# Performance work log

Measured on AMD Instinct MI355X. Metric: run time of the kernel, lower is better.

Reference implementation:

```python
import jax, jax.numpy as jnp
import numpy as np

B, S, D, H, HD = 1, 2048, 1024, 16, 64
GH = 64            # GammaGate hidden dim
FFN_H = int(D * 4 * 2 / 3)
CTX = 512          # omega-rule context window c
LAM = 0.999        # base exponential decay

def _rms(x, w, eps=1e-6):
    return x * jax.lax.rsqrt(jnp.mean(x * x, axis=-1, keepdims=True) + eps) * w

def _rope(q, k):
    hd = q.shape[-1]; s = q.shape[2]
    inv = 1.0 / (10000.0 ** (jnp.arange(0, hd, 2, dtype=jnp.float32) / hd))
    fr = jnp.arange(s, dtype=jnp.float32)[:, None] * inv[None, :]
    cos = jnp.concatenate([jnp.cos(fr), jnp.cos(fr)], -1)
    sin = jnp.concatenate([jnp.sin(fr), jnp.sin(fr)], -1)
    rot = lambda x: jnp.concatenate([-x[..., hd // 2:], x[..., :hd // 2]], -1)
    return q * cos + rot(q) * sin, k * cos + rot(k) * sin

def setup_inputs() -> dict:
    key = jax.random.key(0)
    ks = jax.random.split(key, 10)
    n = lambda i, sh, s=0.02: jax.random.normal(ks[i], sh, jnp.float32) * s
    return dict(
        x=jax.random.normal(ks[0], (B, S, D), jnp.float32),
        norm1_w=jnp.ones((D,), jnp.float32),
        norm2_w=jnp.ones((D,), jnp.float32),
        w_qkv=n(1, (D, 3 * D)),
        q_norm_w=jnp.ones((HD,), jnp.float32),
        k_norm_w=jnp.ones((HD,), jnp.float32),
        gamma_w1=n(2, (D, GH)),
        gamma_w2=n(3, (GH, 1)),
        m_persist=n(4, (H, HD, HD)),
        memory_gate=jnp.array([-3.0], jnp.float32),
        w_o=n(5, (D, D), 0.02 / 2 ** 0.5),
        ffn_w1=n(6, (D, FFN_H)),
        ffn_w3=n(7, (D, FFN_H)),
        ffn_w2=n(8, (FFN_H, D)),
    )

def reference(x, norm1_w, norm2_w, w_qkv, q_norm_w, k_norm_w, gamma_w1, gamma_w2,
              m_persist, memory_gate, w_o, ffn_w1, ffn_w3, ffn_w2):
    b, s, d = x.shape
    h = _rms(x, norm1_w)
    qkv = h @ w_qkv
    q, k, v = jnp.split(qkv, 3, axis=-1)
    rs = lambda t: t.reshape(b, s, H, HD).transpose(0, 2, 1, 3)   # (b,h,s,hd)
    q, k, v = rs(q), rs(k), rs(v)
    q = _rms(q, q_norm_w); k = _rms(k, k_norm_w)                  # qk_norm
    q, k = _rope(q, k)
    # input-dependent gamma gate: Linear->SiLU->Linear->Sigmoid
    gamma = jax.nn.sigmoid(jax.nn.silu(h @ gamma_w1) @ gamma_w2)  # (b,s,1)
    # Omega-rule memory: Q'_t = (M_p q_t + sum_i w_{t,i} k_i (k_i . q_t)) / (1 + sum_i w_{t,i})
    ti = jnp.arange(s)
    delta = ti[:, None] - ti[None, :]
    wmask = (delta >= 0) & (delta < CTX)
    decay = jnp.where(wmask, LAM ** delta.astype(jnp.float32), 0.0)      # (t,i)
    w = decay[None, None] * gamma[:, None, None, :, 0]                   # (b,1,t,i)
    norm = 1.0 + jnp.sum(w, axis=-1)                                     # (b,1,t)
    scores = jnp.einsum('bhtd,bhid->bhti', q, k)
    contrib = jnp.einsum('bhti,bhid->bhtd', w * scores, k)
    persist = jnp.einsum('hde,bhte->bhtd', m_persist, q)
    qp = (persist + contrib) / norm[..., None]
    gate = jax.nn.sigmoid(memory_gate)[0]
    q = (1.0 - gate) * q + gate * qp
    # causal attention
    aw = jnp.einsum('bhtd,bhid->bhti', q, k) * (HD ** -0.5)
    causal = ti[:, None] >= ti[None, :]
    aw = jnp.where(causal[None, None], aw, -jnp.inf)
    aw = jax.nn.softmax(aw, axis=-1)
    ao = jnp.einsum('bhti,bhid->bhtd', aw, v).transpose(0, 2, 1, 3).reshape(b, s, d)
    x = x + ao @ w_o
    h2 = _rms(x, norm2_w)
    x = x + (jax.nn.silu(h2 @ ffn_w1) * (h2 @ ffn_w3)) @ ffn_w2   # SwiGLU
    return x
```

## Files before the change

### kernel.cpp

```cpp
#include <hip/hip_runtime.h>
#include <hip/hip_bf16.h>

#define S_LEN 2048
#define D_DIM 1024
#define H_NUM 16
#define HD_DIM 64
#define GH_DIM 64
#define FFN_H 2730
#define FFNP  2816
#define CTX_W 512
#define L2LAM -0.00144341687f
#define QBLK 64
#define KBLK 64
#define ALDK 76
#define QSCALE 0.1803368801111731f

typedef unsigned short u16;
typedef __attribute__((ext_vector_type(8))) short bf16x8_t;
typedef __attribute__((ext_vector_type(4))) float f32x4_t;

__device__ inline float wave_sum(float v) {
    for (int off = 32; off; off >>= 1) v += __shfl_xor(v, off);
    return v;
}
__device__ inline u16 f2bf(float f) {
    unsigned r;
    asm("v_cvt_pk_bf16_f32 %0, %1, %2" : "=v"(r) : "v"(f), "v"(f));
    return (u16)r;
}
__device__ inline unsigned f2bf2(float lo, float hi) {
    unsigned r;
    asm("v_cvt_pk_bf16_f32 %0, %1, %2" : "=v"(r) : "v"(lo), "v"(hi));
    return r;
}
__device__ inline float bf2f(u16 u) {
    return __uint_as_float(((unsigned int)u) << 16);
}
__device__ inline void gload16(const void* g, void* l) {
    __builtin_amdgcn_global_load_lds(
        (const __attribute__((address_space(1))) void*)g,
        (__attribute__((address_space(3))) void*)l, 16, 0, 0);
}

__global__ __launch_bounds__(256) void rmsnorm_kernel(
    const float* __restrict__ in, const float* __restrict__ w,
    u16* __restrict__ out)
{
    __shared__ float wsum[4];
    int row = blockIdx.x;
    int tid = threadIdx.x, lane = tid & 63, wv = tid >> 6;
    const float4* ir = reinterpret_cast<const float4*>(in + (size_t)row * D_DIM);
    float4 v = ir[tid];
    float ss = v.x*v.x + v.y*v.y + v.z*v.z + v.w*v.w;
    ss = wave_sum(ss);
    if (lane == 0) wsum[wv] = ss;
    __syncthreads();
    float tot = wsum[0] + wsum[1] + wsum[2] + wsum[3];
    float scale = rsqrtf(tot / (float)D_DIM + 1e-6f);
    const float4* wr = reinterpret_cast<const float4*>(w);
    float4 wv4 = wr[tid];
    uint2 o;
    o.x = f2bf2(v.x * scale * wv4.x, v.y * scale * wv4.y);
    o.y = f2bf2(v.z * scale * wv4.z, v.w * scale * wv4.w);
    *reinterpret_cast<uint2*>(out + (size_t)row * D_DIM + tid * 4) = o;
}

__global__ __launch_bounds__(256) void prep_kernel(
    const float* __restrict__ w_qkv, const float* __restrict__ w_o,
    const float* __restrict__ w1f, const float* __restrict__ w3f,
    const float* __restrict__ w2f, const float* __restrict__ gw1f,
    u16* __restrict__ wqT, u16* __restrict__ woT, u16* __restrict__ w13T,
    u16* __restrict__ w2T, u16* __restrict__ gw1T,
    const float* __restrict__ x, const float* __restrict__ norm1_w,
    u16* __restrict__ h_bf)
{
    __shared__ float tile[64][65];
    __shared__ float wsum[4];
    int b = blockIdx.x;
    int tid = threadIdx.x;
    if (b < 3152) {
        const float* src; u16* dst;
        int srcK, srcN, Kp, rowOff, rowMul, nbx;
        if (b < 768)       {           src = w_qkv; dst = wqT;  srcK = 1024; srcN = 3072; Kp = 1024; rowOff = 0; rowMul = 1; nbx = 48; }
        else if (b < 1024) { b -= 768;  src = w_o;  dst = woT;  srcK = 1024; srcN = 1024; Kp = 1024; rowOff = 0; rowMul = 1; nbx = 16; }
        else if (b < 1728) { b -= 1024; src = w1f;  dst = w13T; srcK = 1024; srcN = 2730; Kp = 1024; rowOff = 0; rowMul = 2; nbx = 44; }
        else if (b < 2432) { b -= 1728; src = w3f;  dst = w13T; srcK = 1024; srcN = 2730; Kp = 1024; rowOff = 1; rowMul = 2; nbx = 44; }
        else if (b < 3136) { b -= 2432; src = w2f;  dst = w2T;  srcK = 2730; srcN = 1024; Kp = 2816; rowOff = 0; rowMul = 1; nbx = 16; }
        else               { b -= 3136; src = gw1f; dst = gw1T; srcK = 1024; srcN = 64;   Kp = 1024; rowOff = 0; rowMul = 1; nbx = 1; }
        int n0 = (b % nbx) * 64, k0 = (b / nbx) * 64;
        int tx = tid & 15, ty = tid >> 4;
        bool interior = (k0 + 63 < srcK) && (n0 + 63 < srcN);
        #pragma unroll
        for (int p = 0; p < 4; ++p) {
            int kk = p * 16 + ty;
            int r = k0 + kk;
            int cb = n0 + tx * 4;
            float4 v;
            if (interior) {
                v = *(const float4*)(src + (size_t)r * srcN + cb);
            } else {
                v.x = (r < srcK && cb     < srcN) ? src[(size_t)r * srcN + cb]     : 0.f;
                v.y = (r < srcK && cb + 1 < srcN) ? src[(size_t)r * srcN + cb + 1] : 0.f;
                v.z = (r < srcK && cb + 2 < srcN) ? src[(size_t)r * srcN + cb + 2] : 0.f;
                v.w = (r < srcK && cb + 3 < srcN) ? src[(size_t)r * srcN + cb + 3] : 0.f;
            }
            tile[kk][tx*4+0] = v.x; tile[kk][tx*4+1] = v.y;
            tile[kk][tx*4+2] = v.z; tile[kk][tx*4+3] = v.w;
        }
        __syncthreads();
        int wx = tid & 7, wy = tid >> 3;
        #pragma unroll
        for (int p = 0; p < 2; ++p) {
            int nn = p * 32 + wy;
            int ks = wx * 8;
            uint4 o;
            o.x = f2bf2(tile[ks+0][nn], tile[ks+1][nn]);
            o.y = f2bf2(tile[ks+2][nn], tile[ks+3][nn]);
            o.z = f2bf2(tile[ks+4][nn], tile[ks+5][nn]);
            o.w = f2bf2(tile[ks+6][nn], tile[ks+7][nn]);
            *(uint4*)(dst + (size_t)(rowOff + (size_t)(n0 + nn) * rowMul) * Kp + k0 + ks) = o;
        }
    } else {
        int row = b - 3152;
        int lane = tid & 63, wv = tid >> 6;
        const float4* ir = reinterpret_cast<const float4*>(x + (size_t)row * D_DIM);
        float4 v = ir[tid];
        float ss = v.x*v.x + v.y*v.y + v.z*v.z + v.w*v.w;
        ss = wave_sum(ss);
        if (lane == 0) wsum[wv] = ss;
        __syncthreads();
        float tot = wsum[0] + wsum[1] + wsum[2] + wsum[3];
        float scale = rsqrtf(tot / (float)D_DIM + 1e-6f);
        const float4* wr = reinterpret_cast<const float4*>(norm1_w);
        float4 wv4 = wr[tid];
        uint2 o;
        o.x = f2bf2(v.x * scale * wv4.x, v.y * scale * wv4.y);
        o.y = f2bf2(v.z * scale * wv4.z, v.w * scale * wv4.w);
        *reinterpret_cast<uint2*>(h_bf + (size_t)row * D_DIM + tid * 4) = o;
    }
}

__global__ __launch_bounds__(256) void gamma_gemm_kernel(
    const u16* __restrict__ A, const u16* __restrict__ B,
    const float* __restrict__ w2, float* __restrict__ gamma, int K)
{
    __shared__ u16 As[64 * 64];
    __shared__ u16 Bs[64 * 64];
    __shared__ float red[2][64];
    int tid = threadIdx.x, lane = tid & 63, wid = tid >> 6;
    int wr = wid >> 1, wc = wid & 1;
    int row0 = blockIdx.x * 64;
    int l8 = lane >> 3, l7 = lane & 7;
    f32x4_t acc[2][2];
    #pragma unroll
    for (int i = 0; i < 2; ++i)
        #pragma unroll
        for (int j = 0; j < 2; ++j) acc[i][j] = (f32x4_t)0.f;
    int fr = lane & 15, fo = (lane >> 4) * 8;
    for (int k0 = 0; k0 < K; k0 += 64) {
        #pragma unroll
        for (int i = 0; i < 2; ++i) {
            int ch = wid * 2 + i;
            const u16* ga = A + (size_t)(row0 + ch * 8 + l8) * K + k0 + l7 * 8;
            gload16(ga, &As[ch * 512]);
            const u16* gb = B + (size_t)(ch * 8 + l8) * K + k0 + l7 * 8;
            gload16(gb, &Bs[ch * 512]);
        }
        __syncthreads();
        __builtin_amdgcn_s_setprio(1);
        #pragma unroll
        for (int khf = 0; khf < 2; ++khf) {
            bf16x8_t bfrag[2];
            #pragma unroll
            for (int ni = 0; ni < 2; ++ni)
                bfrag[ni] = *(const bf16x8_t*)&Bs[(wc * 32 + ni * 16 + fr) * 64 + khf * 32 + fo];
            #pragma unroll
            for (int mi = 0; mi < 2; ++mi) {
                bf16x8_t af = *(const bf16x8_t*)&As[(wr * 32 + mi * 16 + fr) * 64 + khf * 32 + fo];
                #pragma unroll
                for (int ni = 0; ni < 2; ++ni)
                    acc[mi][ni] = __builtin_amdgcn_mfma_f32_16x16x32_bf16(
                        af, bfrag[ni], acc[mi][ni], 0, 0, 0);
            }
        }
        __builtin_amdgcn_s_setprio(0);
        __syncthreads();
    }
    int dr = (lane >> 4) * 4, dc = lane & 15;
    float w2v0 = w2[wc * 32 + dc];
    float w2v1 = w2[wc * 32 + 16 + dc];
    #pragma unroll
    for (int mi = 0; mi < 2; ++mi) {
        #pragma unroll
        for (int j = 0; j < 4; ++j) {
            float v0 = acc[mi][0][j];
            float v1 = acc[mi][1][j];
            float t = v0 / (1.f + __expf(-v0)) * w2v0
                    + v1 / (1.f + __expf(-v1)) * w2v1;
            t += __shfl_xor(t, 1);
            t += __shfl_xor(t, 2);
            t += __shfl_xor(t, 4);
            t += __shfl_xor(t, 8);
            if (dc == 0) red[wc][wr * 32 + mi * 16 + dr + j] = t;
        }
    }
    __syncthreads();
    if (tid < 64) {
        float g = red[0][tid] + red[1][tid];
        gamma[row0 + tid] = 1.f / (1.f + __expf(-g));
    }
}

__global__ __launch_bounds__(256) void split_rope_tr_kernel(
    const u16* __restrict__ qkv, const float* __restrict__ qw,
    const float* __restrict__ kw, float* __restrict__ qhp,
    u16* __restrict__ khp, u16* __restrict__ khT, u16* __restrict__ vhT)
{
    __shared__ u16 tk[64][ALDK];
    __shared__ u16 tv[64][ALDK];
    int tid = threadIdx.x;
    int w = tid >> 6, d = tid & 63;
    int h = blockIdx.y;
    int s0 = blockIdx.x * 64;
    float qwv = qw[d], kwv = kw[d];
    int j = d & 31;
    float inv = expf(-(float)j * (9.2103403719761836f / 32.0f));
    float sgn = (d < 32) ? -1.f : 1.f;
    for (int i = 0; i < 16; ++i) {
        int sl = w * 16 + i;
        int s = s0 + sl;
        size_t base = (size_t)s * (3 * D_DIM) + h * HD_DIM + d;
        float qv = bf2f(qkv[base]);
        float kv = bf2f(qkv[base + D_DIM]);
        u16  vv = qkv[base + 2 * D_DIM];
        float sq = wave_sum(qv * qv);
        float qn = qv * rsqrtf(sq / (float)HD_DIM + 1e-6f) * qwv;
        float sk = wave_sum(kv * kv);
        float kn = kv * rsqrtf(sk / (float)HD_DIM + 1e-6f) * kwv;
        float ang = (float)s * inv;
        float cs = cosf(ang), sn = sinf(ang);
        float qp = __shfl_xor(qn, 32);
        float kp = __shfl_xor(kn, 32);
        float qo = qn * cs + sgn * qp * sn;
        float ko = kn * cs + sgn * kp * sn;
        size_t ob = ((size_t)h * S_LEN + s) * HD_DIM + d;
        u16 kb = f2bf(ko);
        qhp[ob] = qo;
        khp[ob] = kb;
        tk[sl][d] = kb;
        tv[sl][d] = vv;
    }
    __syncthreads();
    int r = tid >> 2, cc = (tid & 3) * 16;
    union { u16 u[16]; bf16x8_t v[2]; } ok, ov;
    #pragma unroll
    for (int e = 0; e < 16; ++e) {
        int ksrc = (e & 3) * 16 + (tid & 3) * 4 + (e >> 2);
        ok.u[e] = tk[ksrc][r]; ov.u[e] = tv[ksrc][r];
    }
    u16* kd = khT + ((size_t)h * HD_DIM + r) * S_LEN + s0 + cc;
    u16* vd = vhT + ((size_t)h * HD_DIM + r) * S_LEN + s0 + cc;
    *(bf16x8_t*)kd       = ok.v[0];
    *(bf16x8_t*)(kd + 8) = ok.v[1];
    *(bf16x8_t*)vd       = ov.v[0];
    *(bf16x8_t*)(vd + 8) = ov.v[1];
}

template<int BM, int MODE>
__global__ __launch_bounds__(256) void gemm_bb_kernel(
    const u16* __restrict__ A, const u16* __restrict__ B,
    u16* __restrict__ Cb, int M, int N, int K)
{
    constexpr int MREP = BM / 32;
    constexpr int ACH  = BM / 32;
    __shared__ u16 As[BM * 64];
    __shared__ u16 Bs[128 * 64];
    int tid = threadIdx.x, lane = tid & 63, wid = tid >> 6;
    int wr = wid >> 1, wc = wid & 1;
    int row0 = blockIdx.y * BM, col0 = blockIdx.x * 128;
    int l8 = lane >> 3, l7 = lane & 7;
    f32x4_t acc[MREP][4];
    #pragma unroll
    for (int i = 0; i < MREP; ++i)
        #pragma unroll
        for (int j = 0; j < 4; ++j) acc[i][j] = (f32x4_t)0.f;

    int fr = lane & 15, fo = (lane >> 4) * 8;
    for (int k0 = 0; k0 < K; k0 += 64) {
        #pragma unroll
        for (int i = 0; i < ACH; ++i) {
            int ch = wid * ACH + i;
            const u16* ga = A + (size_t)(row0 + ch * 8 + l8) * K + k0 + l7 * 8;
            gload16(ga, &As[ch * 512]);
        }
        #pragma unroll
        for (int i = 0; i < 4; ++i) {
            int ch = wid * 4 + i;
            const u16* gb = B + (size_t)(col0 + ch * 8 + l8) * K + k0 + l7 * 8;
            gload16(gb, &Bs[ch * 512]);
        }
        __syncthreads();
        __builtin_amdgcn_s_setprio(1);
        #pragma unroll
        for (int khf = 0; khf < 2; ++khf) {
            bf16x8_t bfrag[4];
            #pragma unroll
            for (int ni = 0; ni < 4; ++ni)
                bfrag[ni] = *(const bf16x8_t*)&Bs[(wc * 64 + ni * 16 + fr) * 64 + khf * 32 + fo];
            #pragma unroll
            for (int mi = 0; mi < MREP; ++mi) {
                bf16x8_t af = *(const bf16x8_t*)&As[(wr * (BM / 2) + mi * 16 + fr) * 64 + khf * 32 + fo];
                #pragma unroll
                for (int ni = 0; ni < 4; ++ni)
                    acc[mi][ni] = __builtin_amdgcn_mfma_f32_16x16x32_bf16(
                        af, bfrag[ni], acc[mi][ni], 0, 0, 0);
            }
        }
        __builtin_amdgcn_s_setprio(0);
        __syncthreads();
    }
    int dr = (lane >> 4) * 4, dc = lane & 15;
    #pragma unroll
    for (int mi = 0; mi < MREP; ++mi) {
        int gr = row0 + wr * (BM / 2) + mi * 16 + dr;
        #pragma unroll
        for (int ni = 0; ni < 4; ++ni) {
            int gc = col0 + wc * 64 + ni * 16 + dc;
            #pragma unroll
            for (int j = 0; j < 4; ++j) {
                float v = acc[mi][ni][j];
                if (MODE == 1) {
                    Cb[(size_t)(gr + j) * N + gc] = f2bf(v);
                } else {
                    float partner = __shfl_xor(v, 1);
                    float a1 = (dc & 1) ? partner : v;
                    float a3 = (dc & 1) ? v : partner;
                    float rr = a1 / (1.f + __expf(-a1)) * a3;
                    if (!(dc & 1))
                        Cb[(size_t)(gr + j) * (N >> 1) + (gc >> 1)] = f2bf(rr);
                }
            }
        }
    }
}

__global__ __launch_bounds__(256) void gemm64_kernel(
    const u16* __restrict__ A, const u16* __restrict__ B,
    const float* __restrict__ res, float* __restrict__ Cf,
    int M, int N, int K)
{
    __shared__ u16 As[64 * 64];
    __shared__ u16 Bs[64 * 64];
    int tid = threadIdx.x, lane = tid & 63, wid = tid >> 6;
    int wr = wid >> 1, wc = wid & 1;
    int row0 = blockIdx.y * 64, col0 = blockIdx.x * 64;
    int l8 = lane >> 3, l7 = lane & 7;
    f32x4_t acc[2][2];
    #pragma unroll
    for (int i = 0; i < 2; ++i)
        #pragma unroll
        for (int j = 0; j < 2; ++j) acc[i][j] = (f32x4_t)0.f;
    int fr = lane & 15, fo = (lane >> 4) * 8;
    for (int k0 = 0; k0 < K; k0 += 64) {
        #pragma unroll
        for (int i = 0; i < 2; ++i) {
            int ch = wid * 2 + i;
            const u16* ga = A + (size_t)(row0 + ch * 8 + l8) * K + k0 + l7 * 8;
            gload16(ga, &As[ch * 512]);
            const u16* gb = B + (size_t)(col0 + ch * 8 + l8) * K + k0 + l7 * 8;
            gload16(gb, &Bs[ch * 512]);
        }
        __syncthreads();
        __builtin_amdgcn_s_setprio(1);
        #pragma unroll
        for (int khf = 0; khf < 2; ++khf) {
            bf16x8_t bfrag[2];
            #pragma unroll
            for (int ni = 0; ni < 2; ++ni)
                bfrag[ni] = *(const bf16x8_t*)&Bs[(wc * 32 + ni * 16 + fr) * 64 + khf * 32 + fo];
            #pragma unroll
            for (int mi = 0; mi < 2; ++mi) {
                bf16x8_t af = *(const bf16x8_t*)&As[(wr * 32 + mi * 16 + fr) * 64 + khf * 32 + fo];
                #pragma unroll
                for (int ni = 0; ni < 2; ++ni)
                    acc[mi][ni] = __builtin_amdgcn_mfma_f32_16x16x32_bf16(
                        af, bfrag[ni], acc[mi][ni], 0, 0, 0);
            }
        }
        __builtin_amdgcn_s_setprio(0);
        __syncthreads();
    }
    int dr = (lane >> 4) * 4, dc = lane & 15;
    #pragma unroll
    for (int mi = 0; mi < 2; ++mi) {
        int gr = row0 + wr * 32 + mi * 16 + dr;
        #pragma unroll
        for (int ni = 0; ni < 2; ++ni) {
            int gc = col0 + wc * 32 + ni * 16 + dc;
            #pragma unroll
            for (int j = 0; j < 4; ++j) {
                size_t off = (size_t)(gr + j) * N + gc;
                Cf[off] = acc[mi][ni][j] + res[off];
            }
        }
    }
}

__global__ __launch_bounds__(512) void fused_omega_attn_kernel(
    const float* __restrict__ qhp, const u16* __restrict__ khp,
    const u16* __restrict__ khT, const u16* __restrict__ vhT,
    const float* __restrict__ gammab, const float* __restrict__ mp,
    const float* __restrict__ mg, u16* __restrict__ ao)
{
    __shared__ u16 Ks[2][KBLK][ALDK];
    __shared__ u16 Xt[2][KBLK][ALDK];
    __shared__ u16 Ps[QBLK][ALDK];
    __shared__ float colfL[CTX_W + KBLK];
    __shared__ float redS[2][QBLK];
    const int tid = threadIdx.x, lane = tid & 63, wid = tid >> 6;
    const int wq = wid & 3;
    const int nh = wid >> 2;
    const int b = blockIdx.x;
    const int hi = (b >> 8) & 1;
    const int h = ((b & 7) << 1) + hi;
    const int s5 = (b >> 3) & 31;
    const int qt = hi ? (31 - s5) : s5;
    const int q0 = qt * QBLK;
    const int fr = lane & 15, g4 = lane >> 4;
    const int fko = g4 * 8;
    const int c = fr, rg = g4;
    const int si = tid >> 3, sdb = (tid & 7) * 8;
    const size_t hS = (size_t)h * S_LEN;
    const size_t hD = (size_t)h * HD_DIM;

    int rowt[4]; float rowf[4];
    #pragma unroll
    for (int j = 0; j < 4; ++j) {
        rowt[j] = q0 + wq * 16 + rg * 4 + j;
        rowf[j] = exp2f((float)(wq * 16 + rg * 4 + j) * L2LAM);
    }
    bf16x8_t qf[2];
    {
        const float* qrow = qhp + (hS + q0 + wq * 16 + fr) * HD_DIM;
        #pragma unroll
        for (int u = 0; u < 2; ++u) {
            float4 a = *(const float4*)(qrow + u * 32 + fko);
            float4 bq = *(const float4*)(qrow + u * 32 + fko + 4);
            bf16x8_t f;
            f[0]=f2bf(a.x); f[1]=f2bf(a.y); f[2]=f2bf(a.z); f[3]=f2bf(a.w);
            f[4]=f2bf(bq.x); f[5]=f2bf(bq.y); f[6]=f2bf(bq.z); f[7]=f2bf(bq.w);
            qf[u] = f;
        }
    }
    float qold[2][4];
    #pragma unroll
    for (int nn = 0; nn < 2; ++nn)
        #pragma unroll
        for (int j = 0; j < 4; ++j)
            qold[nn][j] = qhp[(hS + rowt[j]) * HD_DIM + (nh * 2 + nn) * 16 + c];

    f32x4_t accc[2];
    accc[0] = (f32x4_t)0.f; accc[1] = (f32x4_t)0.f;
    float wsum[4] = {0.f, 0.f, 0.f, 0.f};
    const int kt0 = (q0 > (CTX_W - 1)) ? (q0 - (CTX_W - 1)) / KBLK : 0;
    const int i0 = kt0 * KBLK;
    const int nwin = (qt + 1) * KBLK - i0;
    for (int idx = tid; idx < nwin; idx += 512) {
        int icol = i0 + idx;
        colfL[idx] = exp2f((float)(q0 - icol) * L2LAM) * gammab[icol];
    }
    {
        const u16* gk = khp + (hS + kt0 * KBLK + si) * HD_DIM + sdb;
        const u16* gx = khT + (hD + si) * S_LEN + kt0 * KBLK + sdb;
        *(bf16x8_t*)&Ks[0][si][sdb] = *(const bf16x8_t*)gk;
        *(bf16x8_t*)&Xt[0][si][sdb] = *(const bf16x8_t*)gx;
    }
    __syncthreads();
    int cur = 0;
    for (int kt = kt0; kt <= qt; ++kt) {
        const int k0 = kt * KBLK;
        const bool hn = (kt < qt);
        bf16x8_t nk0, nx0;
        if (hn) {
            const u16* gk = khp + (hS + k0 + KBLK + si) * HD_DIM + sdb;
            const u16* gx = khT + (hD + si) * S_LEN + k0 + KBLK + sdb;
            nk0 = *(const bf16x8_t*)gk;
            nx0 = *(const bf16x8_t*)gx;
        }
        f32x4_t s[2];
        s[0] = (f32x4_t)0.f; s[1] = (f32x4_t)0.f;
        __builtin_amdgcn_s_setprio(1);
        #pragma unroll
        for (int u = 0; u < 2; ++u)
            #pragma unroll
            for (int nn = 0; nn < 2; ++nn) {
                bf16x8_t kb = *(const bf16x8_t*)&Ks[cur][(nh * 2 + nn) * 16 + fr][u * 32 + fko];
                s[nn] = __builtin_amdgcn_mfma_f32_16x16x32_bf16(qf[u], kb, s[nn], 0, 0, 0);
            }
        __builtin_amdgcn_s_setprio(0);
        const bool boundary = (kt == kt0) || (kt == qt);
        float colf[2];
        #pragma unroll
        for (int nn = 0; nn < 2; ++nn)
            colf[nn] = colfL[k0 - i0 + (nh * 2 + nn) * 16 + c];
        #pragma unroll
        for (int j = 0; j < 4; ++j) {
            float pv[2];
            #pragma unroll
            for (int nn = 0; nn < 2; ++nn) {
                float w;
                if (boundary) {
                    int delta = rowt[j] - (k0 + (nh * 2 + nn) * 16 + c);
                    w = (delta >= 0 && delta < CTX_W) ? rowf[j] * colf[nn] : 0.f;
                } else {
                    w = rowf[j] * colf[nn];
                }
                wsum[j] += w;
                pv[nn] = w * s[nn][j];
            }
            *(unsigned*)&Ps[wq * 16 + rg * 4 + j][c * 4 + nh * 2] = f2bf2(pv[0], pv[1]);
        }
        __syncthreads();
        __builtin_amdgcn_s_setprio(1);
        #pragma unroll
        for (int u = 0; u < 2; ++u) {
            bf16x8_t pa = *(const bf16x8_t*)&Ps[wq * 16 + fr][u * 32 + fko];
            #pragma unroll
            for (int nn = 0; nn < 2; ++nn) {
                bf16x8_t kb = *(const bf16x8_t*)&Xt[cur][(nh * 2 + nn) * 16 + fr][u * 32 + fko];
                accc[nn] = __builtin_amdgcn_mfma_f32_16x16x32_bf16(pa, kb, accc[nn], 0, 0, 0);
            }
        }
        __builtin_amdgcn_s_setprio(0);
        if (hn) {
            int nxt = cur ^ 1;
            *(bf16x8_t*)&Ks[nxt][si][sdb] = nk0;
            *(bf16x8_t*)&Xt[nxt][si][sdb] = nx0;
        }
        __syncthreads();
        cur ^= 1;
    }
    f32x4_t pacc[2];
    pacc[0] = (f32x4_t)0.f; pacc[1] = (f32x4_t)0.f;
    const float* mph = mp + hD * HD_DIM;
    #pragma unroll
    for (int u = 0; u < 2; ++u)
        #pragma unroll
        for (int nn = 0; nn < 2; ++nn) {
            const float* br = mph + (size_t)((nh * 2 + nn) * 16 + fr) * HD_DIM + u * 32 + fko;
            float4 a = *(const float4*)br;
            float4 bq = *(const float4*)(br + 4);
            bf16x8_t f;
            f[0]=f2bf(a.x); f[1]=f2bf(a.y); f[2]=f2bf(a.z); f[3]=f2bf(a.w);
            f[4]=f2bf(bq.x); f[5]=f2bf(bq.y); f[6]=f2bf(bq.z); f[7]=f2bf(bq.w);
            pacc[nn] = __builtin_amdgcn_mfma_f32_16x16x32_bf16(qf[u], f, pacc[nn], 0, 0, 0);
        }
    #pragma unroll
    for (int j = 0; j < 4; ++j) {
        wsum[j] += __shfl_xor(wsum[j], 1);
        wsum[j] += __shfl_xor(wsum[j], 2);
        wsum[j] += __shfl_xor(wsum[j], 4);
        wsum[j] += __shfl_xor(wsum[j], 8);
    }
    if (fr == 0) {
        #pragma unroll
        for (int j = 0; j < 4; ++j)
            redS[nh][wq * 16 + rg * 4 + j] = wsum[j];
    }
    __syncthreads();
    float wtot[4];
    #pragma unroll
    for (int j = 0; j < 4; ++j)
        wtot[j] = redS[0][wq * 16 + rg * 4 + j] + redS[1][wq * 16 + rg * 4 + j];
    float gate = 1.f / (1.f + __expf(-mg[0]));
    float keep = 1.f - gate;
    #pragma unroll
    for (int nn = 0; nn < 2; ++nn) {
        #pragma unroll
        for (int j = 0; j < 4; ++j) {
            float qn = keep * qold[nn][j] + gate * (pacc[nn][j] + accc[nn][j]) / (1.f + wtot[j]);
            Ps[wq * 16 + rg * 4 + j][(nh * 2 + nn) * 16 + c] = f2bf(qn * QSCALE);
        }
    }
    __syncthreads();
    bf16x8_t qf2[2];
    #pragma unroll
    for (int u = 0; u < 2; ++u)
        qf2[u] = *(const bf16x8_t*)&Ps[wq * 16 + fr][u * 32 + fko];

    f32x4_t acco[2];
    acco[0] = (f32x4_t)0.f; acco[1] = (f32x4_t)0.f;
    float l_run[4] = {0.f, 0.f, 0.f, 0.f};
    {
        const u16* gk = khp + (hS + si) * HD_DIM + sdb;
        const u16* gv = vhT + (hD + si) * S_LEN + sdb;
        *(bf16x8_t*)&Ks[0][si][sdb] = *(const bf16x8_t*)gk;
        *(bf16x8_t*)&Xt[0][si][sdb] = *(const bf16x8_t*)gv;
    }
    __syncthreads();
    cur = 0;
    for (int kt = 0; kt <= qt; ++kt) {
        const int k0 = kt * KBLK;
        const bool hn = (kt < qt);
        bf16x8_t nk0, nv0;
        if (hn) {
            const u16* gk = khp + (hS + k0 + KBLK + si) * HD_DIM + sdb;
            const u16* gv = vhT + (hD + si) * S_LEN + k0 + KBLK + sdb;
            nk0 = *(const bf16x8_t*)gk;
            nv0 = *(const bf16x8_t*)gv;
        }
        f32x4_t s[2];
        s[0] = (f32x4_t)0.f; s[1] = (f32x4_t)0.f;
        __builtin_amdgcn_s_setprio(1);
        #pragma unroll
        for (int u = 0; u < 2; ++u)
            #pragma unroll
            for (int nn = 0; nn < 2; ++nn) {
                bf16x8_t kb = *(const bf16x8_t*)&Ks[cur][(nh * 2 + nn) * 16 + fr][u * 32 + fko];
                s[nn] = __builtin_amdgcn_mfma_f32_16x16x32_bf16(qf2[u], kb, s[nn], 0, 0, 0);
            }
        __builtin_amdgcn_s_setprio(0);
        if (kt == qt) {
            #pragma unroll
            for (int nn = 0; nn < 2; ++nn) {
                int icol = k0 + (nh * 2 + nn) * 16 + c;
                #pragma unroll
                for (int j = 0; j < 4; ++j)
                    if (icol > rowt[j]) s[nn][j] = -1e30f;
            }
        }
        #pragma unroll
        for (int j = 0; j < 4; ++j) {
            float p0 = exp2f(s[0][j]);
            float p1 = exp2f(s[1][j]);
            l_run[j] += p0 + p1;
            *(unsigned*)&Ps[wq * 16 + rg * 4 + j][c * 4 + nh * 2] = f2bf2(p0, p1);
        }
        __syncthreads();
        __builtin_amdgcn_s_setprio(1);
        #pragma unroll
        for (int u = 0; u < 2; ++u) {
            bf16x8_t pa = *(const bf16x8_t*)&Ps[wq * 16 + fr][u * 32 + fko];
            #pragma unroll
            for (int nn = 0; nn < 2; ++nn) {
                bf16x8_t vb = *(const bf16x8_t*)&Xt[cur][(nh * 2 + nn) * 16 + fr][u * 32 + fko];
                acco[nn] = __builtin_amdgcn_mfma_f32_16x16x32_bf16(pa, vb, acco[nn], 0, 0, 0);
            }
        }
        __builtin_amdgcn_s_setprio(0);
        if (hn) {
            int nxt = cur ^ 1;
            *(bf16x8_t*)&Ks[nxt][si][sdb] = nk0;
            *(bf16x8_t*)&Xt[nxt][si][sdb] = nv0;
        }
        __syncthreads();
        cur ^= 1;
    }
    #pragma unroll
    for (int j = 0; j < 4; ++j) {
        l_run[j] += __shfl_xor(l_run[j], 1);
        l_run[j] += __shfl_xor(l_run[j], 2);
        l_run[j] += __shfl_xor(l_run[j], 4);
        l_run[j] += __shfl_xor(l_run[j], 8);
    }
    if (fr == 0) {
        #pragma unroll
        for (int j = 0; j < 4; ++j)
            redS[nh][wq * 16 + rg * 4 + j] = l_run[j];
    }
    __syncthreads();
    #pragma unroll
    for (int j = 0; j < 4; ++j)
        l_run[j] = redS[0][wq * 16 + rg * 4 + j] + redS[1][wq * 16 + rg * 4 + j];
    #pragma unroll
    for (int nn = 0; nn < 2; ++nn) {
        #pragma unroll
        for (int j = 0; j < 4; ++j) {
            float o = acco[nn][j] / l_run[j];
            ao[(size_t)rowt[j] * D_DIM + h * HD_DIM + (nh * 2 + nn) * 16 + c] = f2bf(o);
        }
    }
}

extern "C" void kernel_launch(void* const* d_in, const int* in_sizes, int n_in,
                              void* d_out, int out_size, void* d_ws, size_t ws_size,
                              hipStream_t stream) {
    const float* x         = (const float*)d_in[0];
    const float* norm1_w   = (const float*)d_in[1];
    const float* norm2_w   = (const float*)d_in[2];
    const float* w_qkv     = (const float*)d_in[3];
    const float* q_norm_w  = (const float*)d_in[4];
    const float* k_norm_w  = (const float*)d_in[5];
    const float* gamma_w1  = (const float*)d_in[6];
    const float* gamma_w2  = (const float*)d_in[7];
    const float* m_persist = (const float*)d_in[8];
    const float* mem_gate  = (const float*)d_in[9];
    const float* w_o       = (const float*)d_in[10];
    const float* ffn_w1    = (const float*)d_in[11];
    const float* ffn_w3    = (const float*)d_in[12];
    const float* ffn_w2    = (const float*)d_in[13];
    float* out = (float*)d_out;
    char* ws = (char*)d_ws;

    const size_t MB = 1024 * 1024;
    u16*   h_bf   = (u16*)(ws);
    u16*   wqT    = (u16*)(ws + 4 * MB);
    u16*   woT    = (u16*)(ws + 10 * MB);
    u16*   w13T   = (u16*)(ws + 12 * MB);
    u16*   w2T    = (u16*)(ws + 23 * MB);
    u16*   qkv_bf = (u16*)(ws + 29884416);
    u16*   ao_bf  = (u16*)(ws + 38273024);
    float* qh     = (float*)(ws + 42467328);
    u16*   kh     = (u16*)(ws + 50855936);
    u16*   khT_s  = (u16*)(ws + 50855936 + 4 * MB);
    float* gammab = (float*)(ws + 59244544);
    u16*   vhT_s  = (u16*)(ws + 59244544 + 65536);
    u16*   gw1T   = (u16*)(ws + 63504384);
    u16*   mid_bf = (u16*)(ws + 29884416);

    hipLaunchKernelGGL(prep_kernel, dim3(3152 + S_LEN), dim3(256), 0, stream,
                       w_qkv, w_o, ffn_w1, ffn_w3, ffn_w2, gamma_w1,
                       wqT, woT, w13T, w2T, gw1T, x, norm1_w, h_bf);

    hipLaunchKernelGGL((gemm_bb_kernel<64, 1>), dim3(24, 32), dim3(256), 0, stream,
                       h_bf, wqT, qkv_bf, S_LEN, 3 * D_DIM, D_DIM);
    hipLaunchKernelGGL(gamma_gemm_kernel, dim3(32), dim3(256), 0, stream,
                       h_bf, gw1T, gamma_w2, gammab, D_DIM);
    hipLaunchKernelGGL(split_rope_tr_kernel, dim3(S_LEN / 64, H_NUM), dim3(256), 0, stream,
                       qkv_bf, q_norm_w, k_norm_w, qh, kh, khT_s, vhT_s);
    hipLaunchKernelGGL(fused_omega_attn_kernel, dim3(512), dim3(512), 0, stream,
                       qh, kh, khT_s, vhT_s, gammab, m_persist, mem_gate, ao_bf);
    hipLaunchKernelGGL(gemm64_kernel, dim3(16, 32), dim3(256), 0, stream,
                       ao_bf, woT, x, out, S_LEN, D_DIM, D_DIM);
    hipLaunchKernelGGL(rmsnorm_kernel, dim3(S_LEN), dim3(256), 0, stream,
                       out, norm2_w, h_bf);
    hipLaunchKernelGGL((gemm_bb_kernel<128, 2>), dim3(44, 16), dim3(256), 0, stream,
                       h_bf, w13T, mid_bf, S_LEN, 2 * FFNP, D_DIM);
    hipLaunchKernelGGL(gemm64_kernel, dim3(16, 32), dim3(256), 0, stream,
                       mid_bf, w2T, out, out, S_LEN, D_DIM, FFNP);
}
```

Measured before the change: 217.3 us.

## Move late-use weight transposes into attention kernel to overlap with attention

Transposing and converting the w_o, FFN w1/w3 and w2 weights to bf16 moves out of the up-front prep kernel. It now runs as 2368 extra blocks appended to the fused omega-attention launch, which use 512 threads and reuse the Ks shared buffer as the transpose tile. The goal is to hide this memory-bound conversion inside the tail and idle CU slots of the 512-block attention grid, and to shorten the critical path before the QKV GEMM. The cost is that the extra blocks carry the attention kernel's shared-memory footprint and may compete with attention blocks for bandwidth.

```diff
diff --git a/kernel.cpp b/kernel.cpp
--- a/kernel.cpp
+++ b/kernel.cpp
@@ -66,11 +66,8 @@
 }
 
 __global__ __launch_bounds__(256) void prep_kernel(
-    const float* __restrict__ w_qkv, const float* __restrict__ w_o,
-    const float* __restrict__ w1f, const float* __restrict__ w3f,
-    const float* __restrict__ w2f, const float* __restrict__ gw1f,
-    u16* __restrict__ wqT, u16* __restrict__ woT, u16* __restrict__ w13T,
-    u16* __restrict__ w2T, u16* __restrict__ gw1T,
+    const float* __restrict__ w_qkv, const float* __restrict__ gw1f,
+    u16* __restrict__ wqT, u16* __restrict__ gw1T,
     const float* __restrict__ x, const float* __restrict__ norm1_w,
     u16* __restrict__ h_bf)
 {
@@ -78,15 +75,11 @@
     __shared__ float wsum[4];
     int b = blockIdx.x;
     int tid = threadIdx.x;
-    if (b < 3152) {
+    if (b < 784) {
         const float* src; u16* dst;
-        int srcK, srcN, Kp, rowOff, rowMul, nbx;
-        if (b < 768)       {           src = w_qkv; dst = wqT;  srcK = 1024; srcN = 3072; Kp = 1024; rowOff = 0; rowMul = 1; nbx = 48; }
-        else if (b < 1024) { b -= 768;  src = w_o;  dst = woT;  srcK = 1024; srcN = 1024; Kp = 1024; rowOff = 0; rowMul = 1; nbx = 16; }
-        else if (b < 1728) { b -= 1024; src = w1f;  dst = w13T; srcK = 1024; srcN = 2730; Kp = 1024; rowOff = 0; rowMul = 2; nbx = 44; }
-        else if (b < 2432) { b -= 1728; src = w3f;  dst = w13T; srcK = 1024; srcN = 2730; Kp = 1024; rowOff = 1; rowMul = 2; nbx = 44; }
-        else if (b < 3136) { b -= 2432; src = w2f;  dst = w2T;  srcK = 2730; srcN = 1024; Kp = 2816; rowOff = 0; rowMul = 1; nbx = 16; }
-        else               { b -= 3136; src = gw1f; dst = gw1T; srcK = 1024; srcN = 64;   Kp = 1024; rowOff = 0; rowMul = 1; nbx = 1; }
+        int srcK, srcN, Kp, nbx;
+        if (b < 768) {           src = w_qkv; dst = wqT;  srcK = 1024; srcN = 3072; Kp = 1024; nbx = 48; }
+        else         { b -= 768; src = gw1f;  dst = gw1T; srcK = 1024; srcN = 64;   Kp = 1024; nbx = 1; }
         int n0 = (b % nbx) * 64, k0 = (b / nbx) * 64;
         int tx = tid & 15, ty = tid >> 4;
         bool interior = (k0 + 63 < srcK) && (n0 + 63 < srcN);
@@ -118,10 +111,10 @@
             o.y = f2bf2(tile[ks+2][nn], tile[ks+3][nn]);
             o.z = f2bf2(tile[ks+4][nn], tile[ks+5][nn]);
             o.w = f2bf2(tile[ks+6][nn], tile[ks+7][nn]);
-            *(uint4*)(dst + (size_t)(rowOff + (size_t)(n0 + nn) * rowMul) * Kp + k0 + ks) = o;
+            *(uint4*)(dst + (size_t)(n0 + nn) * Kp + k0 + ks) = o;
         }
     } else {
-        int row = b - 3152;
+        int row = b - 784;
         int lane = tid & 63, wv = tid >> 6;
         const float4* ir = reinterpret_cast<const float4*>(x + (size_t)row * D_DIM);
         float4 v = ir[tid];
@@ -410,7 +403,10 @@
     const float* __restrict__ qhp, const u16* __restrict__ khp,
     const u16* __restrict__ khT, const u16* __restrict__ vhT,
     const float* __restrict__ gammab, const float* __restrict__ mp,
-    const float* __restrict__ mg, u16* __restrict__ ao)
+    const float* __restrict__ mg, u16* __restrict__ ao,
+    const float* __restrict__ w_o, const float* __restrict__ w1f,
+    const float* __restrict__ w3f, const float* __restrict__ w2f,
+    u16* __restrict__ woT, u16* __restrict__ w13T, u16* __restrict__ w2T)
 {
     __shared__ u16 Ks[2][KBLK][ALDK];
     __shared__ u16 Xt[2][KBLK][ALDK];
@@ -418,9 +414,51 @@
     __shared__ float colfL[CTX_W + KBLK];
     __shared__ float redS[2][QBLK];
     const int tid = threadIdx.x, lane = tid & 63, wid = tid >> 6;
+    const int b = blockIdx.x;
+
+    if (b >= 512) {
+        int b2 = b - 512;
+        const float* src; u16* dst;
+        int srcK, srcN, Kp, rowOff, rowMul, nbx;
+        if (b2 < 256)       {             src = w_o; dst = woT;  srcK = 1024; srcN = 1024; Kp = 1024; rowOff = 0; rowMul = 1; nbx = 16; }
+        else if (b2 < 960)  { b2 -= 256;  src = w1f; dst = w13T; srcK = 1024; srcN = 2730; Kp = 1024; rowOff = 0; rowMul = 2; nbx = 44; }
+        else if (b2 < 1664) { b2 -= 960;  src = w3f; dst = w13T; srcK = 1024; srcN = 2730; Kp = 1024; rowOff = 1; rowMul = 2; nbx = 44; }
+        else                { b2 -= 1664; src = w2f; dst = w2T;  srcK = 2730; srcN = 1024; Kp = 2816; rowOff = 0; rowMul = 1; nbx = 16; }
+        int n0 = (b2 % nbx) * 64, k0 = (b2 / nbx) * 64;
+        float* tile = (float*)&Ks[0][0][0];
+        int tx = tid & 15, ty = tid >> 4;
+        bool interior = (k0 + 63 < srcK) && (n0 + 63 < srcN);
+        #pragma unroll
+        for (int p = 0; p < 2; ++p) {
+            int kk = p * 32 + ty;
+            int r = k0 + kk;
+            int cb = n0 + tx * 4;
+            float4 v;
+            if (interior) {
+                v = *(const float4*)(src + (size_t)r * srcN + cb);
+            } else {
+                v.x = (r < srcK && cb     < srcN) ? src[(size_t)r * srcN + cb]     : 0.f;
+                v.y = (r < srcK && cb + 1 < srcN) ? src[(size_t)r * srcN + cb + 1] : 0.f;
+                v.z = (r < srcK && cb + 2 < srcN) ? src[(size_t)r * srcN + cb + 2] : 0.f;
+                v.w = (r < srcK && cb + 3 < srcN) ? src[(size_t)r * srcN + cb + 3] : 0.f;
+            }
+            tile[kk * 65 + tx*4+0] = v.x; tile[kk * 65 + tx*4+1] = v.y;
+            tile[kk * 65 + tx*4+2] = v.z; tile[kk * 65 + tx*4+3] = v.w;
+        }
+        __syncthreads();
+        int wx = tid & 7, wy = tid >> 3;
+        int nn = wy, ks = wx * 8;
+        uint4 o;
+        o.x = f2bf2(tile[(ks+0) * 65 + nn], tile[(ks+1) * 65 + nn]);
+        o.y = f2bf2(tile[(ks+2) * 65 + nn], tile[(ks+3) * 65 + nn]);
+        o.z = f2bf2(tile[(ks+4) * 65 + nn], tile[(ks+5) * 65 + nn]);
+        o.w = f2bf2(tile[(ks+6) * 65 + nn], tile[(ks+7) * 65 + nn]);
+        *(uint4*)(dst + (size_t)(rowOff + (size_t)(n0 + nn) * rowMul) * Kp + k0 + ks) = o;
+        return;
+    }
+
     const int wq = wid & 3;
     const int nh = wid >> 2;
-    const int b = blockIdx.x;
     const int hi = (b >> 8) & 1;
     const int h = ((b & 7) << 1) + hi;
     const int s5 = (b >> 3) & 31;
@@ -718,9 +756,8 @@
     u16*   gw1T   = (u16*)(ws + 63504384);
     u16*   mid_bf = (u16*)(ws + 29884416);
 
-    hipLaunchKernelGGL(prep_kernel, dim3(3152 + S_LEN), dim3(256), 0, stream,
-                       w_qkv, w_o, ffn_w1, ffn_w3, ffn_w2, gamma_w1,
-                       wqT, woT, w13T, w2T, gw1T, x, norm1_w, h_bf);
+    hipLaunchKernelGGL(prep_kernel, dim3(784 + S_LEN), dim3(256), 0, stream,
+                       w_qkv, gamma_w1, wqT, gw1T, x, norm1_w, h_bf);
 
     hipLaunchKernelGGL((gemm_bb_kernel<64, 1>), dim3(24, 32), dim3(256), 0, stream,
                        h_bf, wqT, qkv_bf, S_LEN, 3 * D_DIM, D_DIM);
@@ -728,8 +765,9 @@
                        h_bf, gw1T, gamma_w2, gammab, D_DIM);
     hipLaunchKernelGGL(split_rope_tr_kernel, dim3(S_LEN / 64, H_NUM), dim3(256), 0, stream,
                        qkv_bf, q_norm_w, k_norm_w, qh, kh, khT_s, vhT_s);
-    hipLaunchKernelGGL(fused_omega_attn_kernel, dim3(512), dim3(512), 0, stream,
-                       qh, kh, khT_s, vhT_s, gammab, m_persist, mem_gate, ao_bf);
+    hipLaunchKernelGGL(fused_omega_attn_kernel, dim3(512 + 2368), dim3(512), 0, stream,
+                       qh, kh, khT_s, vhT_s, gammab, m_persist, mem_gate, ao_bf,
+                       w_o, ffn_w1, ffn_w3, ffn_w2, woT, w13T, w2T);
     hipLaunchKernelGGL(gemm64_kernel, dim3(16, 32), dim3(256), 0, stream,
                        ao_bf, woT, x, out, S_LEN, D_DIM, D_DIM);
     hipLaunchKernelGGL(rmsnorm_kernel, dim3(S_LEN), dim3(256), 0, stream,
```

Measured after the change: 207.7 us. 4.4% less time.
